# Kernel tuning notes

Measured on AMD Instinct MI355X. Metric: run time of the kernel, lower is better.

The kernel has to match this reference:

```python
import jax, jax.numpy as jnp
import numpy as np

B, T, DIM, H = 4, 2048, 1024, 16
HD = DIM // H  # 64
ROPE_BASE = 10000.0


def _rope_cos_sin(seq_len, head_dim, dtype):
    # lucidrains rotary-embedding-torch convention: interleaved pairs.
    inv_freq = 1.0 / (ROPE_BASE ** (jnp.arange(0, head_dim, 2, dtype=jnp.float32) / head_dim))
    freqs = jnp.arange(seq_len, dtype=jnp.float32)[:, None] * inv_freq[None, :]  # [T, hd/2]
    freqs = jnp.repeat(freqs, 2, axis=-1)  # [T, hd], each freq duplicated for the pair
    return jnp.cos(freqs).astype(dtype), jnp.sin(freqs).astype(dtype)


def _rotate_half(x):
    # interleaved pairs: (x1, x2) -> (-x2, x1)
    x = x.reshape(*x.shape[:-1], -1, 2)
    x1, x2 = x[..., 0], x[..., 1]
    return jnp.stack([-x2, x1], axis=-1).reshape(*x.shape[:-2], -1)


def _apply_rope(x, cos, sin):
    # x: [B, H, T, hd]; cos/sin: [T, hd]
    return x * cos[None, None, :, :] + _rotate_half(x) * sin[None, None, :, :]


def setup_inputs() -> dict:
    key = jax.random.key(0)
    kx, kqkv, kw, kb = jax.random.split(key, 4)
    s_qkv = 1.0 / np.sqrt(DIM)
    return {
        "x": jax.random.normal(kx, (B, T, DIM), dtype=jnp.float32),
        "w_qkv": jax.random.normal(kqkv, (3 * DIM, DIM), dtype=jnp.float32) * s_qkv,
        "w_proj": jax.random.normal(kw, (DIM, DIM), dtype=jnp.float32) * s_qkv,
        "b_proj": jax.random.normal(kb, (DIM,), dtype=jnp.float32) * 0.01,
    }


def reference(x, w_qkv, w_proj, b_proj):
    b, t, c = x.shape
    qkv = jnp.einsum('btc,dc->btd', x, w_qkv)  # [B, T, 3*C]
    qkv = qkv.reshape(b, t, 3, H, HD).transpose(2, 0, 3, 1, 4)  # [3, B, H, T, hd]
    q, k, v = qkv[0], qkv[1], qkv[2]

    cos, sin = _rope_cos_sin(t, HD, x.dtype)
    q = _apply_rope(q, cos, sin)
    k = _apply_rope(k, cos, sin)

    scale = 1.0 / np.sqrt(HD)
    scores = jnp.einsum('bhqd,bhkd->bhqk', q, k) * scale  # [B, H, T, T]
    attn = jax.nn.softmax(scores, axis=-1)
    out = jnp.einsum('bhqk,bhkd->bhqd', attn, v)  # [B, H, T, hd]

    out = out.transpose(0, 2, 1, 3).reshape(b, t, c)  # [B, T, C]
    return jnp.einsum('btc,dc->btd', out, w_proj) + b_proj
```

## Files before the change

### kernel.cpp

```cpp
#include <hip/hip_runtime.h>
#include <hip/hip_bf16.h>
#include <math.h>

#define Bz   4
#define Tz   2048
#define DIMz 1024
#define Hz   16
#define HDz  64
#define BHz  (Bz*Hz)
#define Mz   (Bz*Tz)
#define LOG2E 1.44269504088896340736f
#define QSCALE (0.125f * LOG2E)

typedef __attribute__((ext_vector_type(8)))  __bf16 bf16x8;
typedef __attribute__((ext_vector_type(4)))  __bf16 bf16x4;
typedef __attribute__((ext_vector_type(2)))  __bf16 bf16x2;
typedef __attribute__((ext_vector_type(4)))  float  f32x4;
typedef __attribute__((ext_vector_type(16))) float  f32x16;

__device__ __forceinline__ f32x4 mfma_16x16x32(bf16x8 a, bf16x8 b, f32x4 c) {
  return __builtin_amdgcn_mfma_f32_16x16x32_bf16(a, b, c, 0, 0, 0);
}
__device__ __forceinline__ f32x16 mfma_32x32x16(bf16x8 a, bf16x8 b, f32x16 c) {
  return __builtin_amdgcn_mfma_f32_32x32x16_bf16(a, b, c, 0, 0, 0);
}

__device__ __forceinline__ ushort f2bf(float f) {
  unsigned u = __float_as_uint(f);
  u += 0x7fffu + ((u >> 16) & 1u);
  return (ushort)(u >> 16);
}
__device__ __forceinline__ float bf2f(ushort h) {
  return __uint_as_float(((unsigned)h) << 16);
}

__device__ __forceinline__ void gl_lds16(const ushort* g, ushort* l) {
  __builtin_amdgcn_global_load_lds(
      (const __attribute__((address_space(1))) unsigned int*)g,
      (__attribute__((address_space(3))) unsigned int*)l, 16, 0, 0);
}

__global__ void k_cvt(const float4* __restrict__ in, ushort4* __restrict__ out, int n4) {
  int i = blockIdx.x * blockDim.x + threadIdx.x;
  if (i >= n4) return;
  float4 v = in[i];
  ushort4 o;
  o.x = f2bf(v.x); o.y = f2bf(v.y); o.z = f2bf(v.z); o.w = f2bf(v.w);
  out[i] = o;
}

__global__ void k_rope_tab(float* __restrict__ tab) {
  int idx = blockIdx.x * blockDim.x + threadIdx.x;
  if (idx >= Tz * 32) return;
  int t = idx >> 5, i = idx & 31;
  double ang = (double)t * exp(((double)(-2 * i) / (double)HDz) * log(10000.0));
  tab[2 * idx]     = (float)cos(ang);
  tab[2 * idx + 1] = (float)sin(ang);
}


__global__ __launch_bounds__(256) void k_gemm_qkv(const ushort* __restrict__ A,
                                                  const ushort* __restrict__ Bw,
                                                  const float* __restrict__ tab,
                                                  ushort* __restrict__ qb,
                                                  ushort* __restrict__ kb,
                                                  ushort* __restrict__ vbt) {
  __shared__ ushort As[128 * 64];
  __shared__ ushort Bs[128 * 64];
  const int tid = threadIdx.x;
  const int bm = (blockIdx.x & 63) << 7;
  const int bn = (blockIdx.x >> 6) << 7;
  const int wid = tid >> 6, lane = tid & 63;
  const int wr = (wid & 1) << 6, wc = (wid >> 1) << 6;
  const int lr = lane & 15, lg = lane >> 4;

  const int r8 = lane >> 3;
  const int cswz = (((lane & 7) ^ r8) << 3);
  const ushort* pA = A  + (size_t)(bm + wid * 8 + r8) * 1024 + cswz;
  const ushort* pB = Bw + (size_t)(bn + wid * 8 + r8) * 1024 + cswz;
  ushort* lA = &As[wid * 512];
  ushort* lB = &Bs[wid * 512];

  const int cs0 = ((lg ^ (lr & 7)) << 3);
  const int cs1 = cs0 ^ 32;

  const f32x4 fz = {0.f, 0.f, 0.f, 0.f};
  f32x4 acc[4][4];
  #pragma unroll
  for (int i = 0; i < 4; i++)
    #pragma unroll
    for (int j = 0; j < 4; j++) acc[i][j] = fz;

  for (int k0 = 0; k0 < 1024; k0 += 64) {
    __syncthreads();
    #pragma unroll
    for (int rep = 0; rep < 4; rep++) {
      gl_lds16(pA + (size_t)rep * 32768 + k0, lA + rep * 2048);
      gl_lds16(pB + (size_t)rep * 32768 + k0, lB + rep * 2048);
    }
    __syncthreads();
    #pragma unroll
    for (int kc = 0; kc < 2; kc++) {
      const int cs = kc ? cs1 : cs0;
      bf16x8 af[4], bfr[4];
      #pragma unroll
      for (int i = 0; i < 4; i++)
        af[i] = *reinterpret_cast<const bf16x8*>(&As[(wr + i * 16 + lr) * 64 + cs]);
      #pragma unroll
      for (int j = 0; j < 4; j++)
        bfr[j] = *reinterpret_cast<const bf16x8*>(&Bs[(wc + j * 16 + lr) * 64 + cs]);
      #pragma unroll
      for (int i = 0; i < 4; i++)
        #pragma unroll
        for (int j = 0; j < 4; j++)
          acc[i][j] = mfma_16x16x32(af[i], bfr[j], acc[i][j]);
    }
  }

  #pragma unroll
  for (int j = 0; j < 4; j++) {
    int col = bn + wc + j * 16 + lr;
    int which = col >> 10;
    int r = col & 1023;
    int h = r >> 6, hd = r & 63;
    #pragma unroll
    for (int i = 0; i < 4; i++) {
      int row0 = bm + wr + i * 16 + lg * 4;
      int b = row0 >> 11, t0 = row0 & 2047;
      if (which == 2) {
        uint lo = (uint)f2bf(acc[i][j][0]) | ((uint)f2bf(acc[i][j][1]) << 16);
        uint hi = (uint)f2bf(acc[i][j][2]) | ((uint)f2bf(acc[i][j][3]) << 16);
        *reinterpret_cast<uint2*>(&vbt[((size_t)(b * Hz + h) * HDz + hd) * Tz + t0]) =
            make_uint2(lo, hi);
      } else {
        ushort* dst = (which == 0) ? qb : kb;
        const float sc = (which == 0) ? QSCALE : 1.0f;
        const float sgn = (hd & 1) ? 1.0f : -1.0f;
        const float* tb = &tab[((size_t)t0 * 32 + (hd >> 1)) * 2];
        #pragma unroll
        for (int q = 0; q < 4; q++) {
          float own = acc[i][j][q];
          float other = __shfl_xor(own, 1);
          float c = tb[q * 64], s = tb[q * 64 + 1];
          dst[(((size_t)(b * Hz + h) * Tz + t0 + q) << 6) + hd] =
              f2bf((own * c + sgn * other * s) * sc);
        }
      }
    }
  }
}

__global__ __launch_bounds__(256, 4) void k_attn(const ushort* __restrict__ qb,
                                                 const ushort* __restrict__ kbp,
                                                 const ushort* __restrict__ vbt,
                                                 ushort* __restrict__ ao) {
  __shared__ ushort Ks[2][64 * 64];
  __shared__ ushort Vs[2][64 * 64];

  const int bid = ((blockIdx.x & 7) << 7) + (blockIdx.x >> 3);
  const int qt = bid & 15;
  const int bh = bid >> 4;
  const int tid = threadIdx.x, wid = tid >> 6, lane = tid & 63;
  const int l31 = lane & 31, hi = lane >> 5;

  const ushort* Kg = kbp + (size_t)bh * Tz * HDz;
  const ushort* Vg = vbt + (size_t)bh * HDz * Tz;

  const ushort* Qrow = qb + ((size_t)bh * Tz + qt * 128 + wid * 32 + l31) * HDz + hi * 8;
  bf16x8 qf[4];
  #pragma unroll
  for (int m = 0; m < 4; m++)
    qf[m] = *reinterpret_cast<const bf16x8*>(Qrow + m * 16);

  bf16x8 onev;
  #pragma unroll
  for (int j = 0; j < 8; j++) onev[j] = (__bf16)1.0f;

  const int r8 = lane >> 3;
  const int c0 = (((lane & 7) ^ r8 ^ ((2 * wid) & 3)) << 3);
  const int c1 = (((lane & 7) ^ r8 ^ ((2 * wid + 1) & 3)) << 3);
  const ushort* kp0 = Kg + (size_t)(wid * 16 + r8) * 64 + c0;
  const ushort* kp1 = Kg + (size_t)(wid * 16 + 8 + r8) * 64 + c1;
  const ushort* vp0 = Vg + (size_t)(wid * 16 + r8) * Tz + c0;
  const ushort* vp1 = Vg + (size_t)(wid * 16 + 8 + r8) * Tz + c1;

  f32x16 oacc0, oacc1, lacc;
  #pragma unroll
  for (int i = 0; i < 16; i++) { oacc0[i] = 0.f; oacc1[i] = 0.f; lacc[i] = 0.f; }

  const int swr = (lane & 7) ^ ((lane >> 3) & 3);
  int csk[4];
  #pragma unroll
  for (int m = 0; m < 4; m++) csk[m] = ((2 * m + hi) ^ swr) << 3;

  union U8 { uint u[4]; bf16x8 v; };

  {
    ushort* kl = &Ks[0][wid * 1024];
    ushort* vl = &Vs[0][wid * 1024];
    gl_lds16(kp0, kl); gl_lds16(kp1, kl + 512);
    gl_lds16(vp0, vl); gl_lds16(vp1, vl + 512);
  }
  __syncthreads();

  int cur = 0;
  for (int kt = 0; kt < Tz / 64; kt++) {
    if (kt + 1 < Tz / 64) {
      ushort* kl = &Ks[cur ^ 1][wid * 1024];
      ushort* vl = &Vs[cur ^ 1][wid * 1024];
      gl_lds16(kp0 + (size_t)(kt + 1) * 4096, kl);
      gl_lds16(kp1 + (size_t)(kt + 1) * 4096, kl + 512);
      gl_lds16(vp0 + (kt + 1) * 64, vl);
      gl_lds16(vp1 + (kt + 1) * 64, vl + 512);
    }

    f32x16 sA, sB;
    #pragma unroll
    for (int i = 0; i < 16; i++) { sA[i] = 0.f; sB[i] = 0.f; }
    __builtin_amdgcn_s_setprio(1);
    #pragma unroll
    for (int m = 0; m < 4; m++) {
      bf16x8 kfA = *reinterpret_cast<const bf16x8*>(&Ks[cur][l31 * 64 + csk[m]]);
      bf16x8 kfB = *reinterpret_cast<const bf16x8*>(&Ks[cur][(32 + l31) * 64 + csk[m]]);
      sA = mfma_32x32x16(kfA, qf[m], sA);
      sB = mfma_32x32x16(kfB, qf[m], sB);
    }
    __builtin_amdgcn_s_setprio(0);

    uint pkA[8], pkB[8];
    #pragma unroll
    for (int i = 0; i < 8; i++) {
      bf16x2 ta, tb2;
      ta[0]  = (__bf16)__builtin_exp2f(sA[2 * i]);
      ta[1]  = (__bf16)__builtin_exp2f(sA[2 * i + 1]);
      tb2[0] = (__bf16)__builtin_exp2f(sB[2 * i]);
      tb2[1] = (__bf16)__builtin_exp2f(sB[2 * i + 1]);
      pkA[i] = *reinterpret_cast<uint*>(&ta);
      pkB[i] = *reinterpret_cast<uint*>(&tb2);
    }

    uint eA0 = __shfl_xor(hi ? pkA[0] : pkA[2], 32);
    uint eA1 = __shfl_xor(hi ? pkA[1] : pkA[3], 32);
    uint eA2 = __shfl_xor(hi ? pkA[4] : pkA[6], 32);
    uint eA3 = __shfl_xor(hi ? pkA[5] : pkA[7], 32);
    uint eB0 = __shfl_xor(hi ? pkB[0] : pkB[2], 32);
    uint eB1 = __shfl_xor(hi ? pkB[1] : pkB[3], 32);
    uint eB2 = __shfl_xor(hi ? pkB[4] : pkB[6], 32);
    uint eB3 = __shfl_xor(hi ? pkB[5] : pkB[7], 32);
    U8 fA0, fA1, fB0, fB1;
    fA0.u[0] = hi ? eA0 : pkA[0]; fA0.u[1] = hi ? eA1 : pkA[1];
    fA0.u[2] = hi ? pkA[2] : eA0; fA0.u[3] = hi ? pkA[3] : eA1;
    fA1.u[0] = hi ? eA2 : pkA[4]; fA1.u[1] = hi ? eA3 : pkA[5];
    fA1.u[2] = hi ? pkA[6] : eA2; fA1.u[3] = hi ? pkA[7] : eA3;
    fB0.u[0] = hi ? eB0 : pkB[0]; fB0.u[1] = hi ? eB1 : pkB[1];
    fB0.u[2] = hi ? pkB[2] : eB0; fB0.u[3] = hi ? pkB[3] : eB1;
    fB1.u[0] = hi ? eB2 : pkB[4]; fB1.u[1] = hi ? eB3 : pkB[5];
    fB1.u[2] = hi ? pkB[6] : eB2; fB1.u[3] = hi ? pkB[7] : eB3;

    __builtin_amdgcn_s_setprio(1);
    lacc = mfma_32x32x16(fA0.v, onev, lacc);
    lacc = mfma_32x32x16(fA1.v, onev, lacc);
    lacc = mfma_32x32x16(fB0.v, onev, lacc);
    lacc = mfma_32x32x16(fB1.v, onev, lacc);
    #pragma unroll
    for (int blk = 0; blk < 2; blk++) {
      const ushort* vrow = &Vs[cur][(blk * 32 + l31) * 64];
      bf16x8 vf0 = *reinterpret_cast<const bf16x8*>(vrow + csk[0]);
      bf16x8 vf1 = *reinterpret_cast<const bf16x8*>(vrow + csk[1]);
      bf16x8 vf2 = *reinterpret_cast<const bf16x8*>(vrow + csk[2]);
      bf16x8 vf3 = *reinterpret_cast<const bf16x8*>(vrow + csk[3]);
      f32x16 o = blk ? oacc1 : oacc0;
      o = mfma_32x32x16(fA0.v, vf0, o);
      o = mfma_32x32x16(fA1.v, vf1, o);
      o = mfma_32x32x16(fB0.v, vf2, o);
      o = mfma_32x32x16(fB1.v, vf3, o);
      if (blk) oacc1 = o; else oacc0 = o;
    }
    __builtin_amdgcn_s_setprio(0);

    __syncthreads();
    cur ^= 1;
  }

  const int b = bh >> 4, h = bh & 15;
  #pragma unroll
  for (int r = 0; r < 16; r++) {
    int qrow = (r & 3) + 8 * (r >> 2) + 4 * hi;
    int t = qt * 128 + wid * 32 + qrow;
    float inv = 1.0f / lacc[r];
    size_t base = ((size_t)(b * Tz + t) * Hz + h) * HDz;
    ao[base + l31]      = f2bf(oacc0[r] * inv);
    ao[base + 32 + l31] = f2bf(oacc1[r] * inv);
  }
}

__global__ __launch_bounds__(256) void k_gemm_proj(const ushort* __restrict__ A,
                                                   const ushort* __restrict__ Bw,
                                                   const float* __restrict__ bias,
                                                   float* __restrict__ out) {
  __shared__ ushort As[128 * 64];
  __shared__ ushort Bs[128 * 64];
  const int tid = threadIdx.x;
  const int bm = (blockIdx.x & 63) << 7;
  const int bn = (blockIdx.x >> 6) << 7;
  const int wid = tid >> 6, lane = tid & 63;
  const int wr = (wid & 1) << 6, wc = (wid >> 1) << 6;
  const int lr = lane & 15, lg = lane >> 4;

  const int r8 = lane >> 3;
  const int cswz = (((lane & 7) ^ r8) << 3);
  const ushort* pA = A  + (size_t)(bm + wid * 8 + r8) * 1024 + cswz;
  const ushort* pB = Bw + (size_t)(bn + wid * 8 + r8) * 1024 + cswz;
  ushort* lA = &As[wid * 512];
  ushort* lB = &Bs[wid * 512];

  const int cs0 = ((lg ^ (lr & 7)) << 3);
  const int cs1 = cs0 ^ 32;

  const f32x4 fz = {0.f, 0.f, 0.f, 0.f};
  f32x4 acc[4][4];
  #pragma unroll
  for (int i = 0; i < 4; i++)
    #pragma unroll
    for (int j = 0; j < 4; j++) acc[i][j] = fz;

  for (int k0 = 0; k0 < 1024; k0 += 64) {
    __syncthreads();
    #pragma unroll
    for (int rep = 0; rep < 4; rep++) {
      gl_lds16(pA + (size_t)rep * 32768 + k0, lA + rep * 2048);
      gl_lds16(pB + (size_t)rep * 32768 + k0, lB + rep * 2048);
    }
    __syncthreads();
    #pragma unroll
    for (int kc = 0; kc < 2; kc++) {
      const int cs = kc ? cs1 : cs0;
      bf16x8 af[4], bfr[4];
      #pragma unroll
      for (int i = 0; i < 4; i++)
        af[i] = *reinterpret_cast<const bf16x8*>(&As[(wr + i * 16 + lr) * 64 + cs]);
      #pragma unroll
      for (int j = 0; j < 4; j++)
        bfr[j] = *reinterpret_cast<const bf16x8*>(&Bs[(wc + j * 16 + lr) * 64 + cs]);
      #pragma unroll
      for (int i = 0; i < 4; i++)
        #pragma unroll
        for (int j = 0; j < 4; j++)
          acc[i][j] = mfma_16x16x32(af[i], bfr[j], acc[i][j]);
    }
  }

  #pragma unroll
  for (int j = 0; j < 4; j++) {
    int col = bn + wc + j * 16 + lr;
    float bv = bias[col];
    #pragma unroll
    for (int i = 0; i < 4; i++) {
      #pragma unroll
      for (int q = 0; q < 4; q++) {
        int row = bm + wr + i * 16 + lg * 4 + q;
        out[(size_t)row * 1024 + col] = acc[i][j][q] + bv;
      }
    }
  }
}

extern "C" void kernel_launch(void* const* d_in, const int* in_sizes, int n_in,
                              void* d_out, int out_size, void* d_ws, size_t ws_size,
                              hipStream_t stream) {
  const float* x      = (const float*)d_in[0];
  const float* w_qkv  = (const float*)d_in[1];
  const float* w_proj = (const float*)d_in[2];
  const float* b_proj = (const float*)d_in[3];
  float* out = (float*)d_out;

  char* ws = (char*)d_ws;
  ushort* xh     = (ushort*)ws; ws += (size_t)Mz * DIMz * 2;
  ushort* wqkvh  = (ushort*)ws; ws += (size_t)3 * DIMz * DIMz * 2;
  ushort* wprojh = (ushort*)ws; ws += (size_t)DIMz * DIMz * 2;
  ushort* qbuf   = (ushort*)ws; ws += (size_t)BHz * Tz * HDz * 2;
  ushort* kbuf   = (ushort*)ws; ws += (size_t)BHz * Tz * HDz * 2;
  ushort* vbuft  = (ushort*)ws; ws += (size_t)BHz * HDz * Tz * 2;
  ushort* aout   = (ushort*)ws; ws += (size_t)Mz * DIMz * 2;
  float*  tab    = (float*)ws;  ws += (size_t)Tz * 32 * 2 * 4;

  k_cvt<<<8192, 256, 0, stream>>>((const float4*)x,      (ushort4*)xh,     Mz * DIMz / 4);
  k_cvt<<<3072, 256, 0, stream>>>((const float4*)w_qkv,  (ushort4*)wqkvh,  3 * DIMz * DIMz / 4);
  k_cvt<<<1024, 256, 0, stream>>>((const float4*)w_proj, (ushort4*)wprojh, DIMz * DIMz / 4);
  k_rope_tab<<<256, 256, 0, stream>>>(tab);
  k_gemm_qkv<<<64 * 24, 256, 0, stream>>>(xh, wqkvh, tab, qbuf, kbuf, vbuft);
  k_attn<<<BHz * (Tz / 128), 256, 0, stream>>>(qbuf, kbuf, vbuft, aout);
  k_gemm_proj<<<64 * 8, 256, 0, stream>>>(aout, wprojh, b_proj, out);
}
```

Baseline: 225.5 us.

## Triple-buffer K, split V prefetch, drop P shuffles, merge convert kernels

```diff
diff --git a/kernel.cpp b/kernel.cpp
--- a/kernel.cpp
+++ b/kernel.cpp
@@ -30,9 +30,6 @@
   u += 0x7fffu + ((u >> 16) & 1u);
   return (ushort)(u >> 16);
 }
-__device__ __forceinline__ float bf2f(ushort h) {
-  return __uint_as_float(((unsigned)h) << 16);
-}
 
 __device__ __forceinline__ void gl_lds16(const ushort* g, ushort* l) {
   __builtin_amdgcn_global_load_lds(
@@ -40,13 +37,22 @@
       (__attribute__((address_space(3))) unsigned int*)l, 16, 0, 0);
 }
 
-__global__ void k_cvt(const float4* __restrict__ in, ushort4* __restrict__ out, int n4) {
+#define N4_X   (Mz * DIMz / 4)
+#define N4_WQ  (3 * DIMz * DIMz / 4)
+#define N4_WP  (DIMz * DIMz / 4)
+__global__ void k_cvt3(const float4* __restrict__ x,  ushort4* __restrict__ ox,
+                       const float4* __restrict__ wq, ushort4* __restrict__ owq,
+                       const float4* __restrict__ wp, ushort4* __restrict__ owp) {
   int i = blockIdx.x * blockDim.x + threadIdx.x;
-  if (i >= n4) return;
-  float4 v = in[i];
+  const float4* in; ushort4* out;
+  if (i < N4_X)                { in = x + i;                 out = ox + i; }
+  else if (i < N4_X + N4_WQ)   { in = wq + (i - N4_X);       out = owq + (i - N4_X); }
+  else if (i < N4_X + N4_WQ + N4_WP) { in = wp + (i - N4_X - N4_WQ); out = owp + (i - N4_X - N4_WQ); }
+  else return;
+  float4 v = *in;
   ushort4 o;
   o.x = f2bf(v.x); o.y = f2bf(v.y); o.z = f2bf(v.z); o.w = f2bf(v.w);
-  out[i] = o;
+  *out = o;
 }
 
 __global__ void k_rope_tab(float* __restrict__ tab) {
@@ -154,8 +160,8 @@
                                                  const ushort* __restrict__ kbp,
                                                  const ushort* __restrict__ vbt,
                                                  ushort* __restrict__ ao) {
-  __shared__ ushort Ks[2][64 * 64];
-  __shared__ ushort Vs[2][64 * 64];
+  __shared__ ushort Ks0[64 * 64], Ks1[64 * 64], Ks2[64 * 64];
+  __shared__ ushort Vs0[64 * 64], Vs1[64 * 64];
 
   const int bid = ((blockIdx.x & 7) << 7) + (blockIdx.x >> 3);
   const int qt = bid & 15;
@@ -192,26 +198,27 @@
   int csk[4];
   #pragma unroll
   for (int m = 0; m < 4; m++) csk[m] = ((2 * m + hi) ^ swr) << 3;
-
-  union U8 { uint u[4]; bf16x8 v; };
-
-  {
-    ushort* kl = &Ks[0][wid * 1024];
-    ushort* vl = &Vs[0][wid * 1024];
-    gl_lds16(kp0, kl); gl_lds16(kp1, kl + 512);
-    gl_lds16(vp0, vl); gl_lds16(vp1, vl + 512);
-  }
-  __syncthreads();
-
-  int cur = 0;
-  for (int kt = 0; kt < Tz / 64; kt++) {
-    if (kt + 1 < Tz / 64) {
-      ushort* kl = &Ks[cur ^ 1][wid * 1024];
-      ushort* vl = &Vs[cur ^ 1][wid * 1024];
-      gl_lds16(kp0 + (size_t)(kt + 1) * 4096, kl);
-      gl_lds16(kp1 + (size_t)(kt + 1) * 4096, kl + 512);
-      gl_lds16(vp0 + (kt + 1) * 64, vl);
-      gl_lds16(vp1 + (kt + 1) * 64, vl + 512);
+  int obv[8];
+  #pragma unroll
+  for (int c = 0; c < 8; c++) obv[c] = ((c ^ swr) << 3) + 4 * hi;
+
+  union FP { uint u[4]; bf16x8 v; };
+  union FV { bf16x4 h[2]; bf16x8 v; };
+
+  ushort *kb_cur = Ks0, *kb_nxt = Ks1, *kb_pre = Ks2;
+  ushort *vb_cur = Vs0, *vb_nxt = Vs1;
+
+  gl_lds16(kp0, kb_cur + wid * 1024); gl_lds16(kp1, kb_cur + wid * 1024 + 512);
+  gl_lds16(kp0 + 4096, kb_nxt + wid * 1024); gl_lds16(kp1 + 4096, kb_nxt + wid * 1024 + 512);
+  gl_lds16(vp0, vb_cur + wid * 1024); gl_lds16(vp1, vb_cur + wid * 1024 + 512);
+  asm volatile("s_waitcnt vmcnt(4)" ::: "memory");
+  __builtin_amdgcn_s_barrier();
+
+  const int NT = Tz / 64;
+  for (int kt = 0; kt < NT; kt++) {
+    if (kt + 2 < NT) {
+      gl_lds16(kp0 + (size_t)(kt + 2) * 4096, kb_pre + wid * 1024);
+      gl_lds16(kp1 + (size_t)(kt + 2) * 4096, kb_pre + wid * 1024 + 512);
     }
 
     f32x16 sA, sB;
@@ -220,42 +227,38 @@
     __builtin_amdgcn_s_setprio(1);
     #pragma unroll
     for (int m = 0; m < 4; m++) {
-      bf16x8 kfA = *reinterpret_cast<const bf16x8*>(&Ks[cur][l31 * 64 + csk[m]]);
-      bf16x8 kfB = *reinterpret_cast<const bf16x8*>(&Ks[cur][(32 + l31) * 64 + csk[m]]);
+      bf16x8 kfA = *reinterpret_cast<const bf16x8*>(&kb_cur[l31 * 64 + csk[m]]);
+      bf16x8 kfB = *reinterpret_cast<const bf16x8*>(&kb_cur[(32 + l31) * 64 + csk[m]]);
       sA = mfma_32x32x16(kfA, qf[m], sA);
       sB = mfma_32x32x16(kfB, qf[m], sB);
     }
     __builtin_amdgcn_s_setprio(0);
 
-    uint pkA[8], pkB[8];
-    #pragma unroll
-    for (int i = 0; i < 8; i++) {
-      bf16x2 ta, tb2;
-      ta[0]  = (__bf16)__builtin_exp2f(sA[2 * i]);
-      ta[1]  = (__bf16)__builtin_exp2f(sA[2 * i + 1]);
-      tb2[0] = (__bf16)__builtin_exp2f(sB[2 * i]);
-      tb2[1] = (__bf16)__builtin_exp2f(sB[2 * i + 1]);
-      pkA[i] = *reinterpret_cast<uint*>(&ta);
-      pkB[i] = *reinterpret_cast<uint*>(&tb2);
-    }
-
-    uint eA0 = __shfl_xor(hi ? pkA[0] : pkA[2], 32);
-    uint eA1 = __shfl_xor(hi ? pkA[1] : pkA[3], 32);
-    uint eA2 = __shfl_xor(hi ? pkA[4] : pkA[6], 32);
-    uint eA3 = __shfl_xor(hi ? pkA[5] : pkA[7], 32);
-    uint eB0 = __shfl_xor(hi ? pkB[0] : pkB[2], 32);
-    uint eB1 = __shfl_xor(hi ? pkB[1] : pkB[3], 32);
-    uint eB2 = __shfl_xor(hi ? pkB[4] : pkB[6], 32);
-    uint eB3 = __shfl_xor(hi ? pkB[5] : pkB[7], 32);
-    U8 fA0, fA1, fB0, fB1;
-    fA0.u[0] = hi ? eA0 : pkA[0]; fA0.u[1] = hi ? eA1 : pkA[1];
-    fA0.u[2] = hi ? pkA[2] : eA0; fA0.u[3] = hi ? pkA[3] : eA1;
-    fA1.u[0] = hi ? eA2 : pkA[4]; fA1.u[1] = hi ? eA3 : pkA[5];
-    fA1.u[2] = hi ? pkA[6] : eA2; fA1.u[3] = hi ? pkA[7] : eA3;
-    fB0.u[0] = hi ? eB0 : pkB[0]; fB0.u[1] = hi ? eB1 : pkB[1];
-    fB0.u[2] = hi ? pkB[2] : eB0; fB0.u[3] = hi ? pkB[3] : eB1;
-    fB1.u[0] = hi ? eB2 : pkB[4]; fB1.u[1] = hi ? eB3 : pkB[5];
-    fB1.u[2] = hi ? pkB[6] : eB2; fB1.u[3] = hi ? pkB[7] : eB3;
+    FP fA0, fA1, fB0, fB1;
+    #pragma unroll
+    for (int i = 0; i < 4; i++) {
+      bf16x2 a0, a1, b0, b1;
+      a0[0] = (__bf16)__builtin_exp2f(sA[2 * i]);
+      a0[1] = (__bf16)__builtin_exp2f(sA[2 * i + 1]);
+      a1[0] = (__bf16)__builtin_exp2f(sA[8 + 2 * i]);
+      a1[1] = (__bf16)__builtin_exp2f(sA[9 + 2 * i]);
+      b0[0] = (__bf16)__builtin_exp2f(sB[2 * i]);
+      b0[1] = (__bf16)__builtin_exp2f(sB[2 * i + 1]);
+      b1[0] = (__bf16)__builtin_exp2f(sB[8 + 2 * i]);
+      b1[1] = (__bf16)__builtin_exp2f(sB[9 + 2 * i]);
+      fA0.u[i] = *reinterpret_cast<uint*>(&a0);
+      fA1.u[i] = *reinterpret_cast<uint*>(&a1);
+      fB0.u[i] = *reinterpret_cast<uint*>(&b0);
+      fB1.u[i] = *reinterpret_cast<uint*>(&b1);
+    }
+
+    asm volatile("s_waitcnt vmcnt(2)" ::: "memory");
+    __builtin_amdgcn_s_barrier();
+
+    if (kt + 1 < NT) {
+      gl_lds16(vp0 + (kt + 1) * 64, vb_nxt + wid * 1024);
+      gl_lds16(vp1 + (kt + 1) * 64, vb_nxt + wid * 1024 + 512);
+    }
 
     __builtin_amdgcn_s_setprio(1);
     lacc = mfma_32x32x16(fA0.v, onev, lacc);
@@ -264,22 +267,27 @@
     lacc = mfma_32x32x16(fB1.v, onev, lacc);
     #pragma unroll
     for (int blk = 0; blk < 2; blk++) {
-      const ushort* vrow = &Vs[cur][(blk * 32 + l31) * 64];
-      bf16x8 vf0 = *reinterpret_cast<const bf16x8*>(vrow + csk[0]);
-      bf16x8 vf1 = *reinterpret_cast<const bf16x8*>(vrow + csk[1]);
-      bf16x8 vf2 = *reinterpret_cast<const bf16x8*>(vrow + csk[2]);
-      bf16x8 vf3 = *reinterpret_cast<const bf16x8*>(vrow + csk[3]);
+      const ushort* vrow = &vb_cur[(blk * 32 + l31) * 64];
+      FV fv0, fv1, fv2, fv3;
+      fv0.h[0] = *reinterpret_cast<const bf16x4*>(vrow + obv[0]);
+      fv0.h[1] = *reinterpret_cast<const bf16x4*>(vrow + obv[1]);
+      fv1.h[0] = *reinterpret_cast<const bf16x4*>(vrow + obv[2]);
+      fv1.h[1] = *reinterpret_cast<const bf16x4*>(vrow + obv[3]);
+      fv2.h[0] = *reinterpret_cast<const bf16x4*>(vrow + obv[4]);
+      fv2.h[1] = *reinterpret_cast<const bf16x4*>(vrow + obv[5]);
+      fv3.h[0] = *reinterpret_cast<const bf16x4*>(vrow + obv[6]);
+      fv3.h[1] = *reinterpret_cast<const bf16x4*>(vrow + obv[7]);
       f32x16 o = blk ? oacc1 : oacc0;
-      o = mfma_32x32x16(fA0.v, vf0, o);
-      o = mfma_32x32x16(fA1.v, vf1, o);
-      o = mfma_32x32x16(fB0.v, vf2, o);
-      o = mfma_32x32x16(fB1.v, vf3, o);
+      o = mfma_32x32x16(fA0.v, fv0.v, o);
+      o = mfma_32x32x16(fA1.v, fv1.v, o);
+      o = mfma_32x32x16(fB0.v, fv2.v, o);
+      o = mfma_32x32x16(fB1.v, fv3.v, o);
       if (blk) oacc1 = o; else oacc0 = o;
     }
     __builtin_amdgcn_s_setprio(0);
 
-    __syncthreads();
-    cur ^= 1;
+    ushort* t0 = kb_cur; kb_cur = kb_nxt; kb_nxt = kb_pre; kb_pre = t0;
+    ushort* t1 = vb_cur; vb_cur = vb_nxt; vb_nxt = t1;
   }
 
   const int b = bh >> 4, h = bh & 15;
@@ -384,9 +392,10 @@
   ushort* aout   = (ushort*)ws; ws += (size_t)Mz * DIMz * 2;
   float*  tab    = (float*)ws;  ws += (size_t)Tz * 32 * 2 * 4;
 
-  k_cvt<<<8192, 256, 0, stream>>>((const float4*)x,      (ushort4*)xh,     Mz * DIMz / 4);
-  k_cvt<<<3072, 256, 0, stream>>>((const float4*)w_qkv,  (ushort4*)wqkvh,  3 * DIMz * DIMz / 4);
-  k_cvt<<<1024, 256, 0, stream>>>((const float4*)w_proj, (ushort4*)wprojh, DIMz * DIMz / 4);
+  k_cvt3<<<(N4_X + N4_WQ + N4_WP + 255) / 256, 256, 0, stream>>>(
+      (const float4*)x, (ushort4*)xh,
+      (const float4*)w_qkv, (ushort4*)wqkvh,
+      (const float4*)w_proj, (ushort4*)wprojh);
   k_rope_tab<<<256, 256, 0, stream>>>(tab);
   k_gemm_qkv<<<64 * 24, 256, 0, stream>>>(xh, wqkvh, tab, qbuf, kbuf, vbuft);
   k_attn<<<BHz * (Tz / 128), 256, 0, stream>>>(qbuf, kbuf, vbuft, aout);
```

Measured after the change: 227.6 us. About the same (+0.9%).
